# Kernel tuning notes

Measured on AMD Instinct MI355X. Metric: run time of the kernel, lower is better.

## Reference

```python
import jax, jax.numpy as jnp
import numpy as np

N_NODES, N_EDGES, NODE_D, EDGE_D, EMB_D, N_GRAPHS = 50000, 800000, 128, 100, 92, 256
N_CONV, FC_D, N_FC, CUTOFF = 3, 128, 2, 6.0


def setup_inputs() -> dict:
    key = jax.random.key(0)
    ks = jax.random.split(key, 24)
    s = 0.05
    inp = {
        "z": jax.random.randint(ks[0], (N_NODES,), 0, 100, dtype=jnp.int32),
        "R": jax.random.normal(ks[1], (N_NODES, 3), dtype=jnp.float32) * 5.0,
        "edge_index": jax.random.randint(ks[2], (2, N_EDGES), 0, N_NODES, dtype=jnp.int32),
        "batch": jnp.sort(jax.random.randint(ks[3], (N_NODES,), 0, N_GRAPHS, dtype=jnp.int32)),
        # learned parameters
        "embedding": jax.random.uniform(ks[4], (100, EMB_D), dtype=jnp.float32),
        "emb_w": jax.random.normal(ks[5], (EMB_D, NODE_D), dtype=jnp.float32) * s,
        "emb_b": jnp.zeros((NODE_D,), jnp.float32),
        "conv_w": jax.random.normal(ks[6], (N_CONV, 2 * NODE_D + EDGE_D, 2 * NODE_D), dtype=jnp.float32) * s,
        "conv_b": jnp.zeros((N_CONV, 2 * NODE_D), jnp.float32),
        "ln_g": jnp.ones((N_CONV, NODE_D), jnp.float32),
        "ln_b": jnp.zeros((N_CONV, NODE_D), jnp.float32),
        "cfc_w": jax.random.normal(ks[7], (NODE_D, FC_D), dtype=jnp.float32) * s,
        "cfc_b": jnp.zeros((FC_D,), jnp.float32),
        "fc_w": jax.random.normal(ks[8], (N_FC, FC_D, FC_D), dtype=jnp.float32) * s,
        "fc_b": jnp.zeros((N_FC, FC_D), jnp.float32),
        "out_w": jax.random.normal(ks[9], (FC_D, 1), dtype=jnp.float32) * s,
        "out_b": jnp.zeros((1,), jnp.float32),
    }
    return inp


def _gaussian_smearing(d):
    offsets = jnp.linspace(0.0, CUTOFF, EDGE_D, dtype=d.dtype)  # [EDGE_D]
    coeff = -0.5 / (offsets[1] - offsets[0]) ** 2
    return jnp.exp(coeff * (d[:, None] - offsets[None, :]) ** 2)  # [E, EDGE_D]


def _layernorm(x, g, b, eps=1e-5):
    mu = x.mean(-1, keepdims=True)
    var = x.var(-1, keepdims=True)
    return (x - mu) / jnp.sqrt(var + eps) * g + b


def reference(z, R, edge_index, batch, embedding, emb_w, emb_b, conv_w, conv_b,
              ln_g, ln_b, cfc_w, cfc_b, fc_w, fc_b, out_w, out_b):
    src, dst = edge_index[0], edge_index[1]  # messages flow src(j) -> dst(i)
    d = jnp.linalg.norm(R[src] - R[dst], axis=-1)  # [E]
    edge_attr = _gaussian_smearing(d)  # [E, EDGE_D]

    x = embedding[z] @ emb_w + emb_b  # [N, NODE_D]
    n = x.shape[0]
    for l in range(conv_w.shape[0]):
        xi, xj = x[dst], x[src]  # gather [E, NODE_D]
        zc = jnp.concatenate([xi, xj, edge_attr], axis=1) @ conv_w[l] + conv_b[l]  # [E, 2*NODE_D]
        z1, z2 = jnp.split(zc, 2, axis=1)
        msg = jax.nn.sigmoid(z1) * jax.nn.softplus(z2)  # [E, NODE_D]
        agg = jax.ops.segment_sum(msg, dst, num_segments=n)  # scatter-add
        x = jax.nn.softplus(_layernorm(agg, ln_g[l], ln_b[l]) + x)

    # global mean pool over graphs
    sums = jax.ops.segment_sum(x, batch, num_segments=N_GRAPHS)
    cnts = jax.ops.segment_sum(jnp.ones((n, 1), x.dtype), batch, num_segments=N_GRAPHS)
    mol = sums / jnp.maximum(cnts, 1.0)  # [N_GRAPHS, NODE_D]

    h = jax.nn.softplus(mol @ cfc_w + cfc_b)
    for l in range(fc_w.shape[0]):
        h = jax.nn.softplus(h @ fc_w[l] + fc_b[l])
    return h @ out_w + out_b  # energy [N_GRAPHS, 1]
```

## Files before the change

kernel.cpp:

```cpp
#include <hip/hip_runtime.h>
#include <hip/hip_bf16.h>
#include <cmath>

#define N_NODES 50000
#define N_EDGES 800000
#define NODE_DIM 128
#define EDGE_DIM 100
#define EMB_DIM 92
#define N_GRAPHS 256

typedef __attribute__((ext_vector_type(8))) short short8_t;
typedef __attribute__((ext_vector_type(4))) float float4_t;

__device__ __forceinline__ float softplus_f(float v) {
    return v > 20.0f ? v : __logf(1.0f + __expf(v));
}
__device__ __forceinline__ float sigmoid_f(float v) {
    return 1.0f / (1.0f + __expf(-v));
}
__device__ __forceinline__ float bflo(unsigned u) { return __uint_as_float(u << 16); }
__device__ __forceinline__ float bfhi(unsigned u) { return __uint_as_float(u & 0xffff0000u); }
__device__ __forceinline__ float hlo(unsigned u) {
    unsigned short s = (unsigned short)(u & 0xffffu);
    _Float16 h; __builtin_memcpy(&h, &s, 2); return (float)h;
}
__device__ __forceinline__ float hhi(unsigned u) {
    unsigned short s = (unsigned short)(u >> 16);
    _Float16 h; __builtin_memcpy(&h, &s, 2); return (float)h;
}

__global__ void deg_kernel(const int* __restrict__ ei, int* __restrict__ deg) {
    int e = blockIdx.x * blockDim.x + threadIdx.x;
    if (e >= N_EDGES) return;
    atomicAdd(&deg[ei[N_EDGES + e]], 1);
}

#define SB 1024
__global__ void scan1_kernel(const int* __restrict__ deg, int* __restrict__ rp,
                             int* __restrict__ bsum) {
    __shared__ int buf[SB];
    int b = blockIdx.x, t = threadIdx.x, i = b * SB + t;
    int v = (i < N_NODES) ? deg[i] : 0;
    buf[t] = v;
    __syncthreads();
    for (int off = 1; off < SB; off <<= 1) {
        int a = (t >= off) ? buf[t - off] : 0;
        __syncthreads();
        buf[t] += a;
        __syncthreads();
    }
    if (i < N_NODES) rp[i] = buf[t] - v;
    if (t == SB - 1) bsum[b] = buf[t];
}
__global__ void scan2_kernel(int* __restrict__ bsum, int n) {
    if (threadIdx.x == 0) {
        int s = 0;
        for (int i = 0; i < n; i++) { int v = bsum[i]; bsum[i] = s; s += v; }
    }
}
__global__ void scan3_kernel(int* __restrict__ rp, const int* __restrict__ bsum) {
    int i = blockIdx.x * SB + threadIdx.x;
    if (i < N_NODES) rp[i] += bsum[blockIdx.x];
    if (i == 0) rp[N_NODES] = N_EDGES;
}

__global__ void fill_kernel(const int* __restrict__ ei, const float* __restrict__ R,
                            const int* __restrict__ row_ptr, int* __restrict__ cnt2,
                            float2* __restrict__ em) {
    int e = blockIdx.x * blockDim.x + threadIdx.x;
    if (e >= N_EDGES) return;
    int s = ei[e];
    int dst = ei[N_EDGES + e];
    float dx = R[3 * s + 0] - R[3 * dst + 0];
    float dy = R[3 * s + 1] - R[3 * dst + 1];
    float dz = R[3 * s + 2] - R[3 * dst + 2];
    float d = sqrtf(dx * dx + dy * dy + dz * dz);
    int pos = row_ptr[dst] + atomicAdd(&cnt2[dst], 1);
    em[pos] = make_float2(__int_as_float(s), d);
}

__global__ void gb_kernel(const int* __restrict__ batch, int* __restrict__ gs) {
    int i = blockIdx.x * 256 + threadIdx.x;
    if (i > N_NODES) return;
    int b = (i < N_NODES) ? batch[i] : N_GRAPHS;
    int pb = (i == 0) ? -1 : batch[i - 1];
    for (int g = pb + 1; g <= b; g++) gs[g] = i;
}

__global__ void wcvt_kernel(const float* __restrict__ conv_w, unsigned* __restrict__ Wep) {
    int i = blockIdx.x * 256 + threadIdx.x;
    if (i >= 3 * EDGE_DIM * 128) return;
    int l = i / (EDGE_DIM * 128), r = i - l * (EDGE_DIM * 128);
    int k = r >> 7, c = r & 127;
    const float* row = conv_w + (size_t)l * 356 * 256 + (size_t)(256 + k) * 256;
    __hip_bfloat16 lo = (__hip_bfloat16)row[c];
    __hip_bfloat16 hi = (__hip_bfloat16)row[128 + c];
    Wep[i] = ((unsigned)*(unsigned short*)&hi << 16) | (unsigned)*(unsigned short*)&lo;
}

__global__ void wprep_kernel(const float* __restrict__ conv_w, short* __restrict__ WbB) {
    int idx = blockIdx.x * 256 + threadIdx.x;
    if (idx >= 3 * 4 * 32 * 64 * 8) return;
    int j = idx & 7;
    int lane = (idx >> 3) & 63;
    int nt = (idx >> 9) & 31;
    int kc = (idx >> 14) & 3;
    int l = idx >> 16;
    int k = kc * 32 + (lane >> 4) * 8 + j;
    int nl = lane & 15;
    int row, col;
    if (nt < 16) { row = k; col = nt * 16 + nl; }
    else { row = 128 + k; col = (nt - 16) * 16 + nl; }
    __hip_bfloat16 bv = (__hip_bfloat16)conv_w[(size_t)l * 356 * 256 + (size_t)row * 256 + col];
    WbB[idx] = *(short*)&bv;
}

__global__ void embed_kernel(const int* __restrict__ z, const float* __restrict__ emb,
                             const float* __restrict__ emb_w, const float* __restrict__ emb_b,
                             float* __restrict__ x, __hip_bfloat16* __restrict__ xb) {
    __shared__ float er[EMB_DIM * 8];
    __shared__ int zi[8];
    int base = blockIdx.x * 8;
    int t = threadIdx.x;
    if (t < 8) zi[t] = z[base + t];
    __syncthreads();
    for (int idx = t; idx < EMB_DIM * 8; idx += 128) {
        int k = idx >> 3, j = idx & 7;
        er[idx] = emb[zi[j] * EMB_DIM + k];
    }
    __syncthreads();
    float acc[8];
    float bb = emb_b[t];
#pragma unroll
    for (int j = 0; j < 8; j++) acc[j] = bb;
    for (int k = 0; k < EMB_DIM; k++) {
        float w = emb_w[k * NODE_DIM + t];
        float4 ja = *(const float4*)&er[k * 8];
        float4 jb = *(const float4*)&er[k * 8 + 4];
        acc[0] = fmaf(w, ja.x, acc[0]); acc[1] = fmaf(w, ja.y, acc[1]);
        acc[2] = fmaf(w, ja.z, acc[2]); acc[3] = fmaf(w, ja.w, acc[3]);
        acc[4] = fmaf(w, jb.x, acc[4]); acc[5] = fmaf(w, jb.y, acc[5]);
        acc[6] = fmaf(w, jb.z, acc[6]); acc[7] = fmaf(w, jb.w, acc[7]);
    }
#pragma unroll
    for (int j = 0; j < 8; j++) {
        x[(base + j) * NODE_DIM + t] = acc[j];
        xb[(base + j) * NODE_DIM + t] = (__hip_bfloat16)acc[j];
    }
}

__global__ __launch_bounds__(256) void node_mfma_kernel(
    const __hip_bfloat16* __restrict__ xb, const short* __restrict__ WbB,
    const float* __restrict__ bl, float* __restrict__ P1f, _Float16* __restrict__ P2h) {
    int t = threadIdx.x;
    int wv = t >> 6, lane = t & 63;
    int mrow = lane & 15, q = lane >> 4;
    int base = blockIdx.x * 16;
    const short* xr = (const short*)xb + (size_t)(base + mrow) * 128 + q * 8;
    float4_t acc[8];
#pragma unroll
    for (int i = 0; i < 8; i++) acc[i] = (float4_t){0.f, 0.f, 0.f, 0.f};
#pragma unroll
    for (int kc = 0; kc < 4; kc++) {
        short8_t a = *(const short8_t*)(xr + kc * 32);
#pragma unroll
        for (int i = 0; i < 8; i++) {
            int nt = wv * 8 + i;
            short8_t b = *(const short8_t*)&WbB[((size_t)(kc * 32 + nt) * 64 + lane) * 8];
            acc[i] = __builtin_amdgcn_mfma_f32_16x16x32_bf16(a, b, acc[i], 0, 0, 0);
        }
    }
#pragma unroll
    for (int i = 0; i < 8; i++) {
        int nt = wv * 8 + i;
        int np = nt * 16 + mrow;
        if (np < 256) {
            float bb = bl[np];
            int off = 2 * (np & 127) + (np >> 7);
#pragma unroll
            for (int r = 0; r < 4; r++)
                P1f[(size_t)(base + q * 4 + r) * 256 + off] = acc[i][r] + bb;
        } else {
            int np2 = np - 256;
            int off = 2 * (np2 & 127) + (np2 >> 7);
#pragma unroll
            for (int r = 0; r < 4; r++)
                P2h[(size_t)(base + q * 4 + r) * 256 + off] = (_Float16)acc[i][r];
        }
    }
}

#define NTAP 10
__device__ __forceinline__ float edge_msg(unsigned bu, float dv, float a1, float a2,
                                          const unsigned* __restrict__ Wc) {
    const float sp_ = 6.0f / 99.0f;
    const float inv_s = 99.0f / 6.0f;
    const float coeff = -0.5f * inv_s * inv_s;
    float z1 = a1 + hlo(bu), z2 = a2 + hhi(bu);
    if (dv <= 6.34f) {
        int k0 = max(0, min(EDGE_DIM - NTAP, (int)ceilf(dv * inv_s - 4.5f)));
        const unsigned* wr = Wc + k0 * 128;
#pragma unroll
        for (int i = 0; i < NTAP; i++) {
            float df = dv - (float)(k0 + i) * sp_;
            float ee = __expf(coeff * df * df);
            unsigned u = wr[i * 128];
            z1 = fmaf(bflo(u), ee, z1);
            z2 = fmaf(bfhi(u), ee, z2);
        }
    }
    return sigmoid_f(z1) * softplus_f(z2);
}

__global__ __launch_bounds__(256) void node_edge_ln_kernel(
    const int* __restrict__ row_ptr, const float2* __restrict__ em,
    const float2* __restrict__ P1p, const unsigned* __restrict__ P2u,
    const unsigned* __restrict__ Wep,
    const float* __restrict__ lg, const float* __restrict__ lb,
    float* __restrict__ x, __hip_bfloat16* __restrict__ xb) {
    int node = blockIdx.x * 2 + (threadIdx.x >> 7);
    int c = threadIdx.x & 127;
    int e0 = row_ptr[node], e1 = row_ptr[node + 1];
    float2 av = P1p[(size_t)node * 128 + c];
    float a1 = av.x, a2 = av.y;
    const unsigned* Wc = Wep + c;
    float acc = 0.f;
    unsigned bA = 0, bB = 0;
    float dvA = 0.f, dvB = 0.f;
    int srcC = 0, srcD = 0;
    float dC = 0.f, dD = 0.f;
    if (e0 < e1) {
        float2 m = em[e0];
        int s = __float_as_int(m.x); dvA = m.y;
        bA = P2u[(size_t)s * 128 + c];
    }
    if (e0 + 1 < e1) {
        float2 m = em[e0 + 1];
        int s = __float_as_int(m.x); dvB = m.y;
        bB = P2u[(size_t)s * 128 + c];
    }
    if (e0 + 2 < e1) { float2 m = em[e0 + 2]; srcC = __float_as_int(m.x); dC = m.y; }
    if (e0 + 3 < e1) { float2 m = em[e0 + 3]; srcD = __float_as_int(m.x); dD = m.y; }
    int e = e0;
    while (e < e1) {
        {
            unsigned b = bA; float dv = dvA;
            if (e + 2 < e1) { bA = P2u[(size_t)srcC * 128 + c]; dvA = dC; }
            if (e + 4 < e1) { float2 m = em[e + 4]; srcC = __float_as_int(m.x); dC = m.y; }
            acc += edge_msg(b, dv, a1, a2, Wc);
        }
        e++;
        if (e >= e1) break;
        {
            unsigned b = bB; float dv = dvB;
            if (e + 2 < e1) { bB = P2u[(size_t)srcD * 128 + c]; dvB = dD; }
            if (e + 4 < e1) { float2 m = em[e + 4]; srcD = __float_as_int(m.x); dD = m.y; }
            acc += edge_msg(b, dv, a1, a2, Wc);
        }
        e++;
    }
    __shared__ float sm[4][2];
    float s1r = acc, s2r = acc * acc;
#pragma unroll
    for (int off = 32; off > 0; off >>= 1) {
        s1r += __shfl_xor(s1r, off);
        s2r += __shfl_xor(s2r, off);
    }
    int wv = threadIdx.x >> 6;
    if ((threadIdx.x & 63) == 0) { sm[wv][0] = s1r; sm[wv][1] = s2r; }
    __syncthreads();
    int w0 = (threadIdx.x >> 7) * 2;
    float S1 = sm[w0][0] + sm[w0 + 1][0];
    float S2 = sm[w0][1] + sm[w0 + 1][1];
    float mu = S1 * (1.0f / 128.0f);
    float var = S2 * (1.0f / 128.0f) - mu * mu;
    float rstd = rsqrtf(fmaxf(var, 0.f) + 1e-5f);
    float xv = x[(size_t)node * 128 + c];
    float res = softplus_f((acc - mu) * rstd * lg[c] + lb[c] + xv);
    x[(size_t)node * 128 + c] = res;
    xb[(size_t)node * 128 + c] = (__hip_bfloat16)res;
}

__global__ void pool_head_kernel(const float* __restrict__ x, const int* __restrict__ gs,
                                 const float* __restrict__ cfc_w, const float* __restrict__ cfc_b,
                                 const float* __restrict__ fc_w, const float* __restrict__ fc_b,
                                 const float* __restrict__ out_w, const float* __restrict__ out_b,
                                 float* __restrict__ out) {
    int g = blockIdx.x, c = threadIdx.x;
    int n0 = gs[g], n1 = gs[g + 1];
    float s = 0.f;
    for (int n = n0; n < n1; n++) s += x[(size_t)n * 128 + c];
    __shared__ float h[128], h2[128];
    h[c] = s / fmaxf((float)(n1 - n0), 1.0f);
    __syncthreads();
    float acc = cfc_b[c];
    for (int k = 0; k < 128; k++) acc = fmaf(h[k], cfc_w[k * 128 + c], acc);
    h2[c] = softplus_f(acc);
    __syncthreads();
    for (int l = 0; l < 2; l++) {
        const float* W = fc_w + l * 128 * 128;
        acc = fc_b[l * 128 + c];
        for (int k = 0; k < 128; k++) acc = fmaf(h2[k], W[k * 128 + c], acc);
        __syncthreads();
        h2[c] = softplus_f(acc);
        __syncthreads();
    }
    h[c] = h2[c] * out_w[c];
    __syncthreads();
    for (int off = 64; off > 0; off >>= 1) {
        if (c < off) h[c] += h[c + off];
        __syncthreads();
    }
    if (c == 0) out[g] = h[0] + out_b[0];
}

extern "C" void kernel_launch(void* const* d_in, const int* in_sizes, int n_in,
                              void* d_out, int out_size, void* d_ws, size_t ws_size,
                              hipStream_t stream) {
    const int*   z      = (const int*)d_in[0];
    const float* R      = (const float*)d_in[1];
    const int*   ei     = (const int*)d_in[2];
    const int*   batch  = (const int*)d_in[3];
    const float* emb    = (const float*)d_in[4];
    const float* emb_w  = (const float*)d_in[5];
    const float* emb_b  = (const float*)d_in[6];
    const float* conv_w = (const float*)d_in[7];
    const float* conv_b = (const float*)d_in[8];
    const float* ln_g   = (const float*)d_in[9];
    const float* ln_b   = (const float*)d_in[10];
    const float* cfc_w  = (const float*)d_in[11];
    const float* cfc_b  = (const float*)d_in[12];
    const float* fc_w   = (const float*)d_in[13];
    const float* fc_b   = (const float*)d_in[14];
    const float* out_w  = (const float*)d_in[15];
    const float* out_b  = (const float*)d_in[16];
    float* out = (float*)d_out;

    float* ws    = (float*)d_ws;
    float* x     = ws;
    float* agg   = x + 6400000;
    float* P1f   = agg + 6400000;
    _Float16* P2h = (_Float16*)(P1f + 12800000);
    float* emf   = (float*)(P2h + 12800000);
    int* s_dst   = (int*)(emf + 1600000);
    int* row_ptr = s_dst + 800000;
    int* deg     = row_ptr + 50004;
    int* cnt2    = deg + 50000;
    int* bsum    = cnt2 + 50000;
    int* gs      = bsum + 64;
    unsigned* Wep        = (unsigned*)(gs + 260);
    short* WbB           = (short*)(Wep + 38400);
    __hip_bfloat16* xb   = (__hip_bfloat16*)(WbB + 196608);
    float2* em = (float2*)emf;

    hipMemsetAsync(deg, 0, (size_t)100000 * 4, stream);
    deg_kernel<<<(N_EDGES + 255) / 256, 256, 0, stream>>>(ei, deg);
    int nsb = (N_NODES + SB - 1) / SB;
    scan1_kernel<<<nsb, SB, 0, stream>>>(deg, row_ptr, bsum);
    scan2_kernel<<<1, 64, 0, stream>>>(bsum, nsb);
    scan3_kernel<<<nsb, SB, 0, stream>>>(row_ptr, bsum);
    fill_kernel<<<(N_EDGES + 255) / 256, 256, 0, stream>>>(ei, R, row_ptr, cnt2, em);
    gb_kernel<<<(N_NODES + 256) / 256 + 1, 256, 0, stream>>>(batch, gs);
    wcvt_kernel<<<(3 * EDGE_DIM * 128 + 255) / 256, 256, 0, stream>>>(conv_w, Wep);
    wprep_kernel<<<(3 * 4 * 32 * 64 * 8 + 255) / 256, 256, 0, stream>>>(conv_w, WbB);

    embed_kernel<<<N_NODES / 8, 128, 0, stream>>>(z, emb, emb_w, emb_b, x, xb);
    for (int l = 0; l < 3; l++) {
        node_mfma_kernel<<<N_NODES / 16, 256, 0, stream>>>(xb, WbB + (size_t)l * 65536,
                                                           conv_b + l * 256, P1f, P2h);
        node_edge_ln_kernel<<<N_NODES / 2, 256, 0, stream>>>(
            row_ptr, em, (const float2*)P1f, (const unsigned*)P2h,
            Wep + (size_t)l * EDGE_DIM * 128,
            ln_g + l * 128, ln_b + l * 128, x, xb);
    }
    pool_head_kernel<<<N_GRAPHS, 128, 0, stream>>>(x, gs, cfc_w, cfc_b, fc_w, fc_b,
                                                   out_w, out_b, out);
}
```

Measured before the change: 992.1 us.

## Process two channels per thread with one wavefront per node in edge kernel

Remaps node_edge_ln_kernel so each 64-lane wavefront handles one node and each lane handles two adjacent channels, using wider vector loads for P1, P2 and the edge-weight taps. Because a whole node now fits in one wavefront, the LayerNorm reduction needs only shuffles and no shared memory or __syncthreads. Per-edge metadata loads and the Gaussian exp work are shared across two channels, roughly halving that overhead. The cost is more registers per thread and fewer threads per node, which lowers latency hiding on the random source gathers.

New measurement: 966.1 us. 2.6% less time.

```diff
diff --git a/kernel.cpp b/kernel.cpp
--- a/kernel.cpp
+++ b/kernel.cpp
@@ -191,94 +191,98 @@
 }
 
 #define NTAP 10
-__device__ __forceinline__ float edge_msg(unsigned bu, float dv, float a1, float a2,
-                                          const unsigned* __restrict__ Wc) {
+__device__ __forceinline__ void edge_msg2(uint2 bu, float dv, float4 a,
+                                          const uint2* __restrict__ Wc,
+                                          float& acc0, float& acc1) {
     const float sp_ = 6.0f / 99.0f;
     const float inv_s = 99.0f / 6.0f;
     const float coeff = -0.5f * inv_s * inv_s;
-    float z1 = a1 + hlo(bu), z2 = a2 + hhi(bu);
+    float z10 = a.x + hlo(bu.x), z20 = a.y + hhi(bu.x);
+    float z11 = a.z + hlo(bu.y), z21 = a.w + hhi(bu.y);
     if (dv <= 6.34f) {
         int k0 = max(0, min(EDGE_DIM - NTAP, (int)ceilf(dv * inv_s - 4.5f)));
-        const unsigned* wr = Wc + k0 * 128;
+        const uint2* wr = Wc + k0 * 64;
 #pragma unroll
         for (int i = 0; i < NTAP; i++) {
             float df = dv - (float)(k0 + i) * sp_;
             float ee = __expf(coeff * df * df);
-            unsigned u = wr[i * 128];
-            z1 = fmaf(bflo(u), ee, z1);
-            z2 = fmaf(bfhi(u), ee, z2);
-        }
-    }
-    return sigmoid_f(z1) * softplus_f(z2);
+            uint2 u = wr[i * 64];
+            z10 = fmaf(bflo(u.x), ee, z10);
+            z20 = fmaf(bfhi(u.x), ee, z20);
+            z11 = fmaf(bflo(u.y), ee, z11);
+            z21 = fmaf(bfhi(u.y), ee, z21);
+        }
+    }
+    acc0 += sigmoid_f(z10) * softplus_f(z20);
+    acc1 += sigmoid_f(z11) * softplus_f(z21);
 }
 
 __global__ __launch_bounds__(256) void node_edge_ln_kernel(
     const int* __restrict__ row_ptr, const float2* __restrict__ em,
-    const float2* __restrict__ P1p, const unsigned* __restrict__ P2u,
-    const unsigned* __restrict__ Wep,
+    const float4* __restrict__ P1q, const uint2* __restrict__ P2q,
+    const uint2* __restrict__ Weq,
     const float* __restrict__ lg, const float* __restrict__ lb,
     float* __restrict__ x, __hip_bfloat16* __restrict__ xb) {
-    int node = blockIdx.x * 2 + (threadIdx.x >> 7);
-    int c = threadIdx.x & 127;
+    int node = blockIdx.x * 4 + (threadIdx.x >> 6);
+    int l = threadIdx.x & 63;
+    int c0 = 2 * l;
     int e0 = row_ptr[node], e1 = row_ptr[node + 1];
-    float2 av = P1p[(size_t)node * 128 + c];
-    float a1 = av.x, a2 = av.y;
-    const unsigned* Wc = Wep + c;
-    float acc = 0.f;
-    unsigned bA = 0, bB = 0;
+    float4 a = P1q[(size_t)node * 64 + l];
+    const uint2* Wc = Weq + l;
+    float acc0 = 0.f, acc1 = 0.f;
+    uint2 bA = make_uint2(0, 0), bB = make_uint2(0, 0);
     float dvA = 0.f, dvB = 0.f;
     int srcC = 0, srcD = 0;
     float dC = 0.f, dD = 0.f;
     if (e0 < e1) {
         float2 m = em[e0];
         int s = __float_as_int(m.x); dvA = m.y;
-        bA = P2u[(size_t)s * 128 + c];
+        bA = P2q[(size_t)s * 64 + l];
     }
     if (e0 + 1 < e1) {
         float2 m = em[e0 + 1];
         int s = __float_as_int(m.x); dvB = m.y;
-        bB = P2u[(size_t)s * 128 + c];
+        bB = P2q[(size_t)s * 64 + l];
     }
     if (e0 + 2 < e1) { float2 m = em[e0 + 2]; srcC = __float_as_int(m.x); dC = m.y; }
     if (e0 + 3 < e1) { float2 m = em[e0 + 3]; srcD = __float_as_int(m.x); dD = m.y; }
     int e = e0;
     while (e < e1) {
         {
-            unsigned b = bA; float dv = dvA;
-            if (e + 2 < e1) { bA = P2u[(size_t)srcC * 128 + c]; dvA = dC; }
+            uint2 b = bA; float dv = dvA;
+            if (e + 2 < e1) { bA = P2q[(size_t)srcC * 64 + l]; dvA = dC; }
             if (e + 4 < e1) { float2 m = em[e + 4]; srcC = __float_as_int(m.x); dC = m.y; }
-            acc += edge_msg(b, dv, a1, a2, Wc);
+            edge_msg2(b, dv, a, Wc, acc0, acc1);
         }
         e++;
         if (e >= e1) break;
         {
-            unsigned b = bB; float dv = dvB;
-            if (e + 2 < e1) { bB = P2u[(size_t)srcD * 128 + c]; dvB = dD; }
+            uint2 b = bB; float dv = dvB;
+            if (e + 2 < e1) { bB = P2q[(size_t)srcD * 64 + l]; dvB = dD; }
             if (e + 4 < e1) { float2 m = em[e + 4]; srcD = __float_as_int(m.x); dD = m.y; }
-            acc += edge_msg(b, dv, a1, a2, Wc);
+            edge_msg2(b, dv, a, Wc, acc0, acc1);
         }
         e++;
     }
-    __shared__ float sm[4][2];
-    float s1r = acc, s2r = acc * acc;
+    float s1 = acc0 + acc1;
+    float s2 = acc0 * acc0 + acc1 * acc1;
 #pragma unroll
     for (int off = 32; off > 0; off >>= 1) {
-        s1r += __shfl_xor(s1r, off);
-        s2r += __shfl_xor(s2r, off);
-    }
-    int wv = threadIdx.x >> 6;
-    if ((threadIdx.x & 63) == 0) { sm[wv][0] = s1r; sm[wv][1] = s2r; }
-    __syncthreads();
-    int w0 = (threadIdx.x >> 7) * 2;
-    float S1 = sm[w0][0] + sm[w0 + 1][0];
-    float S2 = sm[w0][1] + sm[w0 + 1][1];
-    float mu = S1 * (1.0f / 128.0f);
-    float var = S2 * (1.0f / 128.0f) - mu * mu;
+        s1 += __shfl_xor(s1, off);
+        s2 += __shfl_xor(s2, off);
+    }
+    float mu = s1 * (1.0f / 128.0f);
+    float var = s2 * (1.0f / 128.0f) - mu * mu;
     float rstd = rsqrtf(fmaxf(var, 0.f) + 1e-5f);
-    float xv = x[(size_t)node * 128 + c];
-    float res = softplus_f((acc - mu) * rstd * lg[c] + lb[c] + xv);
-    x[(size_t)node * 128 + c] = res;
-    xb[(size_t)node * 128 + c] = (__hip_bfloat16)res;
+    float2 xv = *(const float2*)&x[(size_t)node * 128 + c0];
+    float2 gg = *(const float2*)&lg[c0];
+    float2 bb = *(const float2*)&lb[c0];
+    float r0 = softplus_f((acc0 - mu) * rstd * gg.x + bb.x + xv.x);
+    float r1 = softplus_f((acc1 - mu) * rstd * gg.y + bb.y + xv.y);
+    *(float2*)&x[(size_t)node * 128 + c0] = make_float2(r0, r1);
+    __hip_bfloat16 h0 = (__hip_bfloat16)r0, h1 = (__hip_bfloat16)r1;
+    unsigned pk = ((unsigned)*(unsigned short*)&h1 << 16) | (unsigned)*(unsigned short*)&h0;
+    *(unsigned*)&xb[(size_t)node * 128 + c0] = pk;
 }
 
 __global__ void pool_head_kernel(const float* __restrict__ x, const int* __restrict__ gs,
@@ -368,9 +372,9 @@
     for (int l = 0; l < 3; l++) {
         node_mfma_kernel<<<N_NODES / 16, 256, 0, stream>>>(xb, WbB + (size_t)l * 65536,
                                                            conv_b + l * 256, P1f, P2h);
-        node_edge_ln_kernel<<<N_NODES / 2, 256, 0, stream>>>(
-            row_ptr, em, (const float2*)P1f, (const unsigned*)P2h,
-            Wep + (size_t)l * EDGE_DIM * 128,
+        node_edge_ln_kernel<<<N_NODES / 4, 256, 0, stream>>>(
+            row_ptr, em, (const float4*)P1f, (const uint2*)P2h,
+            (const uint2*)(Wep + (size_t)l * EDGE_DIM * 128),
             ln_g + l * 128, ln_b + l * 128, x, xb);
     }
     pool_head_kernel<<<N_GRAPHS, 128, 0, stream>>>(x, gs, cfc_w, cfc_b, fc_w, fc_b,
```
